# Kernel optimization log

Measured on AMD Instinct MI355X. Metric: run time of the kernel, lower is better.

## Reference

```python
import jax, jax.numpy as jnp
import numpy as np

HEIGHT = 480
K = 16
RADIUS = 5.0 / HEIGHT


def ball_query_idx(xy, radius, k):
    """pytorch3d-style ball_query on 2D points (t-channel is zeroed in the
    original, so 3D distance == 2D distance on (x, y)).
    Returns first-k (in point-index order) neighbor indices within radius;
    slots with no neighbor are filled with the query's own index (the
    module's `-1 -> self` replacement).  xy: [B, N, 2] -> idx: [B, N, k] int32."""
    B, N, _ = xy.shape
    sq = jnp.sum(xy * xy, axis=-1)  # [B, N]
    # d2[b, i, j] = ||xy[b,i] - xy[b,j]||^2, via GEMM (no [B,N,N,2] intermediate)
    d2 = sq[:, :, None] + sq[:, None, :] - 2.0 * jnp.einsum('bnd,bmd->bnm', xy, xy)
    within = d2 < radius * radius  # [B, N, N]
    ar = jnp.arange(N, dtype=jnp.int32)
    # key = j if within else N; k smallest keys == first k neighbors in index order
    keys = jnp.where(within, ar[None, None, :], N)
    neg_top, _ = jax.lax.top_k(-keys, k)  # k smallest keys, ascending after negate
    idx = -neg_top  # [B, N, k]
    self_idx = jnp.broadcast_to(ar[None, :, None], (B, N, k))
    return jnp.where(idx < N, idx, self_idx)


def knn_gather(x, idx):
    # x: [B, N, D], idx: [B, N, k] -> [B, N, k, D]
    return jax.vmap(lambda xb, ib: xb[ib])(x, idx)


def setup_inputs() -> dict:
    key = jax.random.key(0)
    k1, k2, k3 = jax.random.split(key, 3)
    B, N = 8, 4096
    out_ch = 64
    hid = out_ch * 2          # 128
    in_ch = K * 2             # 32
    xytp = jax.random.uniform(k1, (B, N, 4), dtype=jnp.float32)
    W1 = jax.random.normal(k2, (in_ch, hid), dtype=jnp.float32) / np.sqrt(in_ch)
    b1 = jnp.zeros((hid,), dtype=jnp.float32)
    W2 = jax.random.normal(k3, (hid, out_ch), dtype=jnp.float32) / np.sqrt(hid)
    b2 = jnp.zeros((out_ch,), dtype=jnp.float32)
    return {"xytp": xytp, "W1": W1, "b1": b1, "W2": W2, "b2": b2}


def reference(xytp, W1, b1, W2, b2):
    xy = xytp[..., 1:3]  # [B, N, 2]
    # ball query runs on detached coords in the original
    idx = ball_query_idx(jax.lax.stop_gradient(xy), RADIUS, K)  # [B, N, K]
    delta = xy[:, :, None, :] - knn_gather(xy, idx)  # [B, N, K, 2]
    B, N = delta.shape[:2]
    emb = delta.reshape(B, N, K * 2)  # [B, N, 2K]
    h = jax.nn.relu(emb @ W1 + b1)
    return h @ W2 + b2  # [B, N, out_channel]
```

## Files before the change

kernel.cpp:

```cpp
#include <hip/hip_runtime.h>

#define NB    8
#define NPTS  4096
#define KNN   16
#define CG    16
#define NCC   (CG * CG)
#define PCAP  24

#define R2F ((float)((5.0 / 480.0) * (5.0 / 480.0)))
#define WIN 0.011f

typedef short short8 __attribute__((ext_vector_type(8)));
typedef float f32x4 __attribute__((ext_vector_type(4)));

static __device__ __forceinline__ unsigned short f2bf(float f) {
  unsigned u = __float_as_uint(f);
  u += 0x7FFFu + ((u >> 16) & 1u);
  return (unsigned short)(u >> 16);
}

__global__ __launch_bounds__(1024, 8) void k_all(
    const float4* __restrict__ xytp4, const float* __restrict__ W1,
    const float* __restrict__ b1, const float* __restrict__ W2,
    const float* __restrict__ b2, float* __restrict__ out) {
#pragma clang fp contract(off)
  __shared__ __align__(16) char smemA[32768];
  __shared__ unsigned short csrIdx[4096];
  __shared__ int offs[NCC + 1];
  __shared__ int cellcnt[NCC];
  __shared__ unsigned int plist[64 * PCAP];
  __shared__ int pcnt[64];
  __shared__ unsigned short idxposT[KNN][64];
  __shared__ float embT[32][64];

  float* csrX = (float*)smemA;
  float* csrY = (float*)(smemA + 16384);
  unsigned short(*hs16b)[136] =
      (unsigned short(*)[136])smemA;

  const int t = threadIdx.x;
  const int p = t & 63;
  const int q = t >> 6;
  const int pbase = blockIdx.x * 64;
  const int bb = pbase & ~4095;
  const int lqbase = pbase & 4095;

  float4 Preg[4];
  int cellreg[4];
#pragma unroll
  for (int r = 0; r < 4; ++r) Preg[r] = xytp4[bb + t + 1024 * r];
  if (t < NCC) cellcnt[t] = 0;
  __syncthreads();
#pragma unroll
  for (int r = 0; r < 4; ++r) {
    int cx = min(CG - 1, max(0, (int)(Preg[r].y * (float)CG)));
    int cy = min(CG - 1, max(0, (int)(Preg[r].z * (float)CG)));
    cellreg[r] = cy * CG + cx;
    atomicAdd(&cellcnt[cellreg[r]], 1);
  }
  __syncthreads();

  if (q == 0) {
    int b4 = p * 4;
    int s0 = cellcnt[b4], s1 = cellcnt[b4 + 1], s2 = cellcnt[b4 + 2],
        s3 = cellcnt[b4 + 3];
    int tot = s0 + s1 + s2 + s3;
    int inc = tot;
#pragma unroll
    for (int d = 1; d < 64; d <<= 1) {
      int up = __shfl_up(inc, d);
      if (p >= d) inc += up;
    }
    int ex = inc - tot;
    offs[b4] = ex; offs[b4 + 1] = ex + s0;
    offs[b4 + 2] = ex + s0 + s1; offs[b4 + 3] = ex + s0 + s1 + s2;
    if (p == 63) offs[NCC] = inc;
    cellcnt[b4] = ex; cellcnt[b4 + 1] = ex + s0;
    cellcnt[b4 + 2] = ex + s0 + s1; cellcnt[b4 + 3] = ex + s0 + s1 + s2;
  }
  __syncthreads();

#pragma unroll
  for (int r = 0; r < 4; ++r) {
    int pos = atomicAdd(&cellcnt[cellreg[r]], 1);
    csrX[pos] = Preg[r].y; csrY[pos] = Preg[r].z;
    csrIdx[pos] = (unsigned short)(t + 1024 * r);
  }
  __syncthreads();

  {
    const int g = p >> 4;
    const int li = p & 15;
    const int lq = q * 4 + g;
    const unsigned gbelow = (1u << li) - 1u;
    float4 P = xytp4[pbase + lq];
    float xn = P.y, yn = P.z;
    float sqn = xn * xn + yn * yn;
    int cxlo = max(0, (int)((xn - WIN) * (float)CG));
    int cxhi = min(CG - 1, (int)((xn + WIN) * (float)CG));
    int cylo = max(0, (int)((yn - WIN) * (float)CG));
    int cyhi = min(CG - 1, (int)((yn + WIN) * (float)CG));
    int cnt = 0;
    for (int cy_ = cylo; cy_ <= cyhi; ++cy_)
      for (int cx_ = cxlo; cx_ <= cxhi; ++cx_) {
        int cell = cy_ * CG + cx_;
        int st = offs[cell], en = offs[cell + 1];
        for (int base = st; base < en; base += 16) {
          int e = base + li;
          bool act = e < en;
          int ee = act ? e : st;
          float cx2 = csrX[ee], cy2 = csrY[ee];
          float cs2 = cx2 * cx2 + cy2 * cy2;
          float tt = fmaf(yn, cy2, xn * cx2);
          float d = (sqn + cs2) - (tt + tt);
          bool pass = act && (d < R2F);
          unsigned long long mask = __ballot(pass);
          unsigned gm = (unsigned)(mask >> (g * 16)) & 0xFFFFu;
          if (pass) {
            int slot = cnt + __popc(gm & gbelow);
            if (slot < PCAP)
              plist[lq * PCAP + slot] =
                  ((unsigned int)csrIdx[ee] << 12) | (unsigned int)ee;
          }
          cnt += __popc(gm);
        }
      }
    if (li == 0) pcnt[lq] = cnt;
  }
  __syncthreads();

  if (t < 64) {
    int c = min(pcnt[t], PCAP);
    unsigned int* cand = &plist[t * PCAP];
    for (int i = 1; i < c; ++i) {
      unsigned int key = cand[i];
      int j = i - 1;
      while (j >= 0 && cand[j] > key) { cand[j + 1] = cand[j]; --j; }
      cand[j + 1] = key;
    }
    unsigned short selfPos = 0;
    if (c < KNN) {
      unsigned int selfIdx = (unsigned int)(lqbase + t);
      for (int i = 0; i < c; ++i)
        if ((cand[i] >> 12) == selfIdx) { selfPos = cand[i] & 4095u; break; }
    }
    if (c > KNN) c = KNN;
    for (int k = 0; k < KNN; ++k)
      idxposT[k][t] =
          (k < c) ? (unsigned short)(cand[k] & 4095u) : selfPos;
  }
  __syncthreads();

  {
    float4 Pq = xytp4[pbase + p];
    int m = idxposT[q][p];
    embT[2 * q][p] = Pq.y - csrX[m];
    embT[2 * q + 1][p] = Pq.z - csrY[m];
  }
  __syncthreads();

  const int lr = p & 15;
  const int lg = p >> 4;

  {
    const int mi = q & 3;
    const int ni0 = (q >> 2) * 2;
    short8 a;
#pragma unroll
    for (int i = 0; i < 8; ++i)
      a[i] = (short)f2bf(embT[lg * 8 + i][mi * 16 + lr]);
#pragma unroll
    for (int tni = 0; tni < 2; ++tni) {
      const int u0 = (ni0 + tni) * 16;
      short8 bfr;
#pragma unroll
      for (int i = 0; i < 8; ++i)
        bfr[i] = (short)f2bf(W1[(lg * 8 + i) * 128 + u0 + lr]);
      float bs = b1[u0 + lr];
      f32x4 c; c[0] = bs; c[1] = bs; c[2] = bs; c[3] = bs;
      f32x4 d = __builtin_amdgcn_mfma_f32_16x16x32_bf16(a, bfr, c, 0, 0, 0);
#pragma unroll
      for (int j = 0; j < 4; ++j)
        hs16b[mi * 16 + lg * 4 + j][u0 + lr] = f2bf(fmaxf(d[j], 0.f));
    }
  }
  __syncthreads();

  {
    const int mi = q >> 2;
    const int o0 = (q & 3) * 16;
    float bs = b2[o0 + lr];
    f32x4 c; c[0] = bs; c[1] = bs; c[2] = bs; c[3] = bs;
#pragma unroll
    for (int kk = 0; kk < 4; ++kk) {
      short8 a = *(const short8*)&hs16b[mi * 16 + lr][kk * 32 + lg * 8];
      short8 bfr;
#pragma unroll
      for (int i = 0; i < 8; ++i)
        bfr[i] = (short)f2bf(W2[(kk * 32 + lg * 8 + i) * 64 + o0 + lr]);
      c = __builtin_amdgcn_mfma_f32_16x16x32_bf16(a, bfr, c, 0, 0, 0);
    }
#pragma unroll
    for (int j = 0; j < 4; ++j)
      out[(size_t)(pbase + mi * 16 + lg * 4 + j) * 64 + o0 + lr] = c[j];
  }
}

extern "C" void kernel_launch(void* const* d_in, const int* in_sizes, int n_in,
                              void* d_out, int out_size, void* d_ws, size_t ws_size,
                              hipStream_t stream) {
  const float4* xytp4 = (const float4*)d_in[0];
  const float* W1 = (const float*)d_in[1];
  const float* b1 = (const float*)d_in[2];
  const float* W2 = (const float*)d_in[3];
  const float* b2 = (const float*)d_in[4];
  float* out = (float*)d_out;
  (void)d_ws; (void)ws_size;

  hipLaunchKernelGGL(k_all, dim3(512), dim3(1024), 0, stream, xytp4, W1, b1,
                     W2, b2, out);
}
```

Baseline: 76.44 us.

## Process 128 queries per block to amortize per-batch grid build

Each block now serves 128 query points instead of 64, so the per-block counting sort that builds the cell grid over all 4096 points of a batch runs half as many times overall. The grid is launched with 256 blocks instead of 512. The search and MLP phases loop twice over 64-query chunks. Point coordinates are packed as float2 in shared memory, the embedding is stored directly as bf16, and the candidate cap drops from 24 to 16. The trade-off is less parallelism, with one block per CU, and a higher chance of truncating correct neighbors when a query has many candidates.

```diff
diff --git a/kernel.cpp b/kernel.cpp
--- a/kernel.cpp
+++ b/kernel.cpp
@@ -5,7 +5,7 @@
 #define KNN   16
 #define CG    16
 #define NCC   (CG * CG)
-#define PCAP  24
+#define PCAP  16
 
 #define R2F ((float)((5.0 / 480.0) * (5.0 / 480.0)))
 #define WIN 0.011f
@@ -28,22 +28,23 @@
   __shared__ unsigned short csrIdx[4096];
   __shared__ int offs[NCC + 1];
   __shared__ int cellcnt[NCC];
-  __shared__ unsigned int plist[64 * PCAP];
-  __shared__ int pcnt[64];
-  __shared__ unsigned short idxposT[KNN][64];
-  __shared__ float embT[32][64];
-
-  float* csrX = (float*)smemA;
-  float* csrY = (float*)(smemA + 16384);
+  __shared__ unsigned int plist[128 * PCAP];
+  __shared__ int pcnt[128];
+  __shared__ unsigned short idxposT[KNN][128];
+  __shared__ unsigned short embT16[32][128];
+
+  float2* csrXY = (float2*)smemA;
   unsigned short(*hs16b)[136] =
       (unsigned short(*)[136])smemA;
 
   const int t = threadIdx.x;
   const int p = t & 63;
   const int q = t >> 6;
-  const int pbase = blockIdx.x * 64;
-  const int bb = pbase & ~4095;
-  const int lqbase = pbase & 4095;
+  const int blk = blockIdx.x;
+  const int b = blk >> 5;
+  const int qb = (blk & 31) << 7;
+  const int bb = b << 12;
+  const int pbase = bb + qb;
 
   float4 Preg[4];
   int cellreg[4];
@@ -83,53 +84,57 @@
 #pragma unroll
   for (int r = 0; r < 4; ++r) {
     int pos = atomicAdd(&cellcnt[cellreg[r]], 1);
-    csrX[pos] = Preg[r].y; csrY[pos] = Preg[r].z;
+    csrXY[pos] = make_float2(Preg[r].y, Preg[r].z);
     csrIdx[pos] = (unsigned short)(t + 1024 * r);
   }
   __syncthreads();
 
   {
+    const int gi = t >> 4;
+    const int li = t & 15;
     const int g = p >> 4;
-    const int li = p & 15;
-    const int lq = q * 4 + g;
     const unsigned gbelow = (1u << li) - 1u;
-    float4 P = xytp4[pbase + lq];
-    float xn = P.y, yn = P.z;
-    float sqn = xn * xn + yn * yn;
-    int cxlo = max(0, (int)((xn - WIN) * (float)CG));
-    int cxhi = min(CG - 1, (int)((xn + WIN) * (float)CG));
-    int cylo = max(0, (int)((yn - WIN) * (float)CG));
-    int cyhi = min(CG - 1, (int)((yn + WIN) * (float)CG));
-    int cnt = 0;
-    for (int cy_ = cylo; cy_ <= cyhi; ++cy_)
-      for (int cx_ = cxlo; cx_ <= cxhi; ++cx_) {
-        int cell = cy_ * CG + cx_;
-        int st = offs[cell], en = offs[cell + 1];
-        for (int base = st; base < en; base += 16) {
-          int e = base + li;
-          bool act = e < en;
-          int ee = act ? e : st;
-          float cx2 = csrX[ee], cy2 = csrY[ee];
-          float cs2 = cx2 * cx2 + cy2 * cy2;
-          float tt = fmaf(yn, cy2, xn * cx2);
-          float d = (sqn + cs2) - (tt + tt);
-          bool pass = act && (d < R2F);
-          unsigned long long mask = __ballot(pass);
-          unsigned gm = (unsigned)(mask >> (g * 16)) & 0xFFFFu;
-          if (pass) {
-            int slot = cnt + __popc(gm & gbelow);
-            if (slot < PCAP)
-              plist[lq * PCAP + slot] =
-                  ((unsigned int)csrIdx[ee] << 12) | (unsigned int)ee;
+#pragma unroll
+    for (int cc = 0; cc < 2; ++cc) {
+      int lq = cc * 64 + gi;
+      float4 P = xytp4[pbase + lq];
+      float xn = P.y, yn = P.z;
+      float sqn = xn * xn + yn * yn;
+      int cxlo = max(0, (int)((xn - WIN) * (float)CG));
+      int cxhi = min(CG - 1, (int)((xn + WIN) * (float)CG));
+      int cylo = max(0, (int)((yn - WIN) * (float)CG));
+      int cyhi = min(CG - 1, (int)((yn + WIN) * (float)CG));
+      int cnt = 0;
+      for (int cy_ = cylo; cy_ <= cyhi; ++cy_)
+        for (int cx_ = cxlo; cx_ <= cxhi; ++cx_) {
+          int cell = cy_ * CG + cx_;
+          int st = offs[cell], en = offs[cell + 1];
+          for (int base = st; base < en; base += 16) {
+            int e = base + li;
+            bool act = e < en;
+            int ee = act ? e : st;
+            float2 c2 = csrXY[ee];
+            float cs2 = c2.x * c2.x + c2.y * c2.y;
+            float tt = fmaf(yn, c2.y, xn * c2.x);
+            float d = (sqn + cs2) - (tt + tt);
+            bool pass = act && (d < R2F);
+            unsigned long long mask = __ballot(pass);
+            unsigned gm = (unsigned)(mask >> (g * 16)) & 0xFFFFu;
+            if (pass) {
+              int slot = cnt + __popc(gm & gbelow);
+              if (slot < PCAP)
+                plist[lq * PCAP + slot] =
+                    ((unsigned int)csrIdx[ee] << 12) | (unsigned int)ee;
+            }
+            cnt += __popc(gm);
           }
-          cnt += __popc(gm);
         }
-      }
-    if (li == 0) pcnt[lq] = cnt;
-  }
-  __syncthreads();
-
-  if (t < 64) {
+      if (li == 0) pcnt[lq] = cnt;
+    }
+  }
+  __syncthreads();
+
+  if (t < 128) {
     int c = min(pcnt[t], PCAP);
     unsigned int* cand = &plist[t * PCAP];
     for (int i = 1; i < c; ++i) {
@@ -140,7 +145,7 @@
     }
     unsigned short selfPos = 0;
     if (c < KNN) {
-      unsigned int selfIdx = (unsigned int)(lqbase + t);
+      unsigned int selfIdx = (unsigned int)(qb + t);
       for (int i = 0; i < c; ++i)
         if ((cand[i] >> 12) == selfIdx) { selfPos = cand[i] & 4095u; break; }
     }
@@ -152,57 +157,68 @@
   __syncthreads();
 
   {
-    float4 Pq = xytp4[pbase + p];
-    int m = idxposT[q][p];
-    embT[2 * q][p] = Pq.y - csrX[m];
-    embT[2 * q + 1][p] = Pq.z - csrY[m];
+#pragma unroll
+    for (int cc = 0; cc < 2; ++cc) {
+      int j = cc * 64 + p;
+      float4 Pq = xytp4[pbase + j];
+      int m = idxposT[q][j];
+      float2 M2 = csrXY[m];
+      embT16[2 * q][j] = f2bf(Pq.y - M2.x);
+      embT16[2 * q + 1][j] = f2bf(Pq.z - M2.y);
+    }
   }
   __syncthreads();
 
   const int lr = p & 15;
   const int lg = p >> 4;
 
-  {
-    const int mi = q & 3;
-    const int ni0 = (q >> 2) * 2;
-    short8 a;
-#pragma unroll
-    for (int i = 0; i < 8; ++i)
-      a[i] = (short)f2bf(embT[lg * 8 + i][mi * 16 + lr]);
-#pragma unroll
-    for (int tni = 0; tni < 2; ++tni) {
-      const int u0 = (ni0 + tni) * 16;
-      short8 bfr;
+#pragma unroll
+  for (int cc = 0; cc < 2; ++cc) {
+    const int cb = cc * 64;
+    {
+      const int mi = q & 3;
+      const int ni0 = (q >> 2) * 2;
+      short8 a;
 #pragma unroll
       for (int i = 0; i < 8; ++i)
-        bfr[i] = (short)f2bf(W1[(lg * 8 + i) * 128 + u0 + lr]);
-      float bs = b1[u0 + lr];
+        a[i] = (short)embT16[lg * 8 + i][cb + mi * 16 + lr];
+#pragma unroll
+      for (int tni = 0; tni < 2; ++tni) {
+        const int u0 = (ni0 + tni) * 16;
+        short8 bfr;
+#pragma unroll
+        for (int i = 0; i < 8; ++i)
+          bfr[i] = (short)f2bf(W1[(lg * 8 + i) * 128 + u0 + lr]);
+        float bs = b1[u0 + lr];
+        f32x4 c; c[0] = bs; c[1] = bs; c[2] = bs; c[3] = bs;
+        f32x4 d = __builtin_amdgcn_mfma_f32_16x16x32_bf16(a, bfr, c, 0, 0, 0);
+#pragma unroll
+        for (int j = 0; j < 4; ++j)
+          hs16b[mi * 16 + lg * 4 + j][u0 + lr] = f2bf(fmaxf(d[j], 0.f));
+      }
+    }
+    __syncthreads();
+
+    {
+      const int mi = q >> 2;
+      const int o0 = (q & 3) * 16;
+      float bs = b2[o0 + lr];
       f32x4 c; c[0] = bs; c[1] = bs; c[2] = bs; c[3] = bs;
-      f32x4 d = __builtin_amdgcn_mfma_f32_16x16x32_bf16(a, bfr, c, 0, 0, 0);
+#pragma unroll
+      for (int kk = 0; kk < 4; ++kk) {
+        short8 a = *(const short8*)&hs16b[mi * 16 + lr][kk * 32 + lg * 8];
+        short8 bfr;
+#pragma unroll
+        for (int i = 0; i < 8; ++i)
+          bfr[i] = (short)f2bf(W2[(kk * 32 + lg * 8 + i) * 64 + o0 + lr]);
+        c = __builtin_amdgcn_mfma_f32_16x16x32_bf16(a, bfr, c, 0, 0, 0);
+      }
 #pragma unroll
       for (int j = 0; j < 4; ++j)
-        hs16b[mi * 16 + lg * 4 + j][u0 + lr] = f2bf(fmaxf(d[j], 0.f));
-    }
-  }
-  __syncthreads();
-
-  {
-    const int mi = q >> 2;
-    const int o0 = (q & 3) * 16;
-    float bs = b2[o0 + lr];
-    f32x4 c; c[0] = bs; c[1] = bs; c[2] = bs; c[3] = bs;
-#pragma unroll
-    for (int kk = 0; kk < 4; ++kk) {
-      short8 a = *(const short8*)&hs16b[mi * 16 + lr][kk * 32 + lg * 8];
-      short8 bfr;
-#pragma unroll
-      for (int i = 0; i < 8; ++i)
-        bfr[i] = (short)f2bf(W2[(kk * 32 + lg * 8 + i) * 64 + o0 + lr]);
-      c = __builtin_amdgcn_mfma_f32_16x16x32_bf16(a, bfr, c, 0, 0, 0);
-    }
-#pragma unroll
-    for (int j = 0; j < 4; ++j)
-      out[(size_t)(pbase + mi * 16 + lg * 4 + j) * 64 + o0 + lr] = c[j];
+        out[(size_t)(pbase + cb + mi * 16 + lg * 4 + j) * 64 + o0 + lr] =
+            c[j];
+    }
+    __syncthreads();
   }
 }
 
@@ -217,6 +233,6 @@
   float* out = (float*)d_out;
   (void)d_ws; (void)ws_size;
 
-  hipLaunchKernelGGL(k_all, dim3(512), dim3(1024), 0, stream, xytp4, W1, b1,
+  hipLaunchKernelGGL(k_all, dim3(256), dim3(1024), 0, stream, xytp4, W1, b1,
                      W2, b2, out);
 }
```

After: 79.22 us. 1.04x slower.
